# Performance work log

Hardware: AMD Instinct MI355X
Metric: run time of the kernel (lower is better)

Reference implementation:

```python
import jax, jax.numpy as jnp
import numpy as np

BN_EPS = 1e-5


def sparsemax_lastdim(z):
    # simplex projection along last axis (Martins & Astudillo 2016)
    zs = -jnp.sort(-z, axis=-1)                      # descending sort
    L = z.shape[-1]
    k = jnp.arange(1, L + 1, dtype=z.dtype)          # [L]
    cum = jnp.cumsum(zs, axis=-1)
    support = (1.0 + k * zs) > cum                   # bool [.., L]
    k_sup = jnp.sum(support, axis=-1, keepdims=True).astype(z.dtype)
    tau = (jnp.sum(jnp.where(support, zs, 0.0), axis=-1, keepdims=True) - 1.0) / k_sup
    return jnp.maximum(z - tau, 0.0)


def setup_inputs() -> dict:
    key = jax.random.key(0)
    k1, k2, k3, k4 = jax.random.split(key, 4)
    B, C_in, C_out, L, K = 16, 256, 256, 8192, 3
    x = jax.random.normal(k1, (B, C_in, L), dtype=jnp.float32)
    bn_weight = jax.random.uniform(k2, (C_in,), dtype=jnp.float32)
    bn_bias = jax.random.normal(k3, (C_in,), dtype=jnp.float32) * 0.1
    v = jax.random.normal(k4, (C_out, C_in, K), dtype=jnp.float32) * 0.05
    g = jnp.asarray(1.0, dtype=jnp.float32)  # weight_norm dim=None -> scalar gain
    return {"x": x, "bn_weight": bn_weight, "bn_bias": bn_bias, "v": v, "g": g}


def reference(x, bn_weight, bn_bias, v, g):
    # BatchNorm1d (training mode: batch statistics over batch and length)
    mean = jnp.mean(x, axis=(0, 2), keepdims=True)           # [1,C,1]
    var = jnp.mean((x - mean) ** 2, axis=(0, 2), keepdims=True)
    xn = (x - mean) * jax.lax.rsqrt(var + BN_EPS)
    xn = xn * bn_weight[None, :, None] + bn_bias[None, :, None]
    # Sparsemax over last (length) dim
    s = sparsemax_lastdim(xn)
    # weight-norm Conv1d (dim=None: scalar g over full Frobenius norm), no bias
    w = g * v / jnp.sqrt(jnp.sum(v * v))                      # [O,I,K]
    y = jax.lax.conv_general_dilated(
        s, w, window_strides=(1,), padding=[(1, 1)],
        dimension_numbers=("NCH", "OIH", "NCH"))
    # ReLU
    return jnp.maximum(y, 0.0)
```

## Files before the change

### kernel.cpp

```cpp
#include <hip/hip_runtime.h>
#include <stdint.h>
#include <math.h>

#define B_ 16
#define C_ 256
#define O_ 256
#define L_ 8192
#define NBL (B_*L_)
#define EPS_ 1e-5

typedef unsigned short ushort_t;
typedef _Float16 f16x8 __attribute__((ext_vector_type(8)));
typedef float f32x4 __attribute__((ext_vector_type(4)));

__device__ inline float wred_f(float v) {
#pragma unroll
    for (int o = 32; o > 0; o >>= 1) v += __shfl_down(v, o, 64);
    return v;
}
__device__ inline int wred_i(int v) {
#pragma unroll
    for (int o = 32; o > 0; o >>= 1) v += __shfl_down(v, o, 64);
    return v;
}
__device__ inline double wred_d(double v) {
#pragma unroll
    for (int o = 32; o > 0; o >>= 1) v += __shfl_down(v, o, 64);
    return v;
}

__device__ inline ushort_t f16bits(float x) {
    union { _Float16 h; ushort_t u; } c; c.h = (_Float16)x; return c.u;
}

__global__ __launch_bounds__(256) void k_bnpart(const float* __restrict__ x,
                                                double* __restrict__ pS,
                                                double* __restrict__ pS2) {
    const int bid = blockIdx.x;
    const int c = bid >> 2;
    const int part = bid & 3;
    const int tid = threadIdx.x;
    const int lane = tid & 63, w = tid >> 6;
    double s = 0.0, s2 = 0.0;
#pragma unroll
    for (int b = 0; b < 4; ++b) {
        const float4* p = (const float4*)(x + ((size_t)(part * 4 + b) * C_ + c) * L_);
#pragma unroll
        for (int j = 0; j < 8; ++j) {
            float4 q = p[j * 256 + tid];
            s  += (double)q.x + (double)q.y + (double)q.z + (double)q.w;
            s2 += (double)q.x * q.x + (double)q.y * q.y + (double)q.z * q.z + (double)q.w * q.w;
        }
    }
    s = wred_d(s); s2 = wred_d(s2);
    __shared__ double sv[4], sv2[4];
    if (lane == 0) { sv[w] = s; sv2[w] = s2; }
    __syncthreads();
    if (tid == 0) {
        pS[bid]  = sv[0] + sv[1] + sv[2] + sv[3];
        pS2[bid] = sv2[0] + sv2[1] + sv2[2] + sv2[3];
    }
}

__global__ __launch_bounds__(256) void k_vpart(const float* __restrict__ v,
                                               double* __restrict__ pv) {
    const int tid = threadIdx.x;
    const float4 q = ((const float4*)v)[(size_t)blockIdx.x * 256 + tid];
    double s2 = (double)q.x * q.x + (double)q.y * q.y + (double)q.z * q.z + (double)q.w * q.w;
    s2 = wred_d(s2);
    __shared__ double sv[4];
    const int lane = tid & 63, w = tid >> 6;
    if (lane == 0) sv[w] = s2;
    __syncthreads();
    if (tid == 0) pv[blockIdx.x] = sv[0] + sv[1] + sv[2] + sv[3];
}

__global__ __launch_bounds__(256) void k_finalize(const float* __restrict__ gamma,
                                                  const float* __restrict__ beta,
                                                  const float* __restrict__ g,
                                                  const double* __restrict__ pS,
                                                  const double* __restrict__ pS2,
                                                  const double* __restrict__ pv,
                                                  float* __restrict__ ab,
                                                  float* __restrict__ invn) {
    const int tid = threadIdx.x;
    const int lane = tid & 63, w = tid >> 6;
    double s2 = (tid < 192) ? pv[tid] : 0.0;
    s2 = wred_d(s2);
    __shared__ double sv[4];
    if (lane == 0) sv[w] = s2;
    __syncthreads();
    if (tid == 0) invn[0] = (float)((double)g[0] / sqrt(sv[0] + sv[1] + sv[2] + sv[3]));

    const int c = tid;
    double s  = pS[c * 4] + pS[c * 4 + 1] + pS[c * 4 + 2] + pS[c * 4 + 3];
    double ss = pS2[c * 4] + pS2[c * 4 + 1] + pS2[c * 4 + 2] + pS2[c * 4 + 3];
    const double N = (double)NBL;
    double mean = s / N;
    double var = ss / N - mean * mean;
    double rstd = 1.0 / sqrt(var + EPS_);
    double a = (double)gamma[c] * rstd;
    ab[c] = (float)a;
    ab[C_ + c] = (float)((double)beta[c] - mean * a);
}

__global__ __launch_bounds__(256) void k_wprep(const float* __restrict__ v,
                                               const float* __restrict__ invn,
                                               ushort_t* __restrict__ W,
                                               ushort_t* __restrict__ zp8) {
    const int o = blockIdx.x;
    const int c = threadIdx.x;
    const float sc = invn[0];
    if (blockIdx.x == 0) {
        for (int i = threadIdx.x; i < 4608; i += 256) zp8[i] = 0;
    }
#pragma unroll
    for (int tap = 0; tap < 3; ++tap) {
        float w = v[((size_t)o * C_ + c) * 3 + tap] * sc;
        int idx = ((tap * 16 + (o >> 4)) * 32 + (c >> 3)) * 128 + (o & 15) * 8 + (c & 7);
        W[idx] = f16bits(w);
    }
}

__global__ __launch_bounds__(256) void k_tau(const float* __restrict__ x,
                                             const float* __restrict__ ab,
                                             float* __restrict__ tauv) {
    const int row = blockIdx.x;
    const int c = row & (C_ - 1);
    const int tid = threadIdx.x;
    const int lane = tid & 63, w = tid >> 6;
    __shared__ float svf[4];
    __shared__ int svi[4];
    __shared__ float s_tau;
    __shared__ int s_cnt;

    const float a = ab[c];
    const float bb = ab[C_ + c];
    const float4* px = (const float4*)(x + (size_t)row * L_);

    float z[32];
    float sm = 0.f;
#pragma unroll
    for (int j = 0; j < 8; ++j) {
        float4 q = px[j * 256 + tid];
        float z0 = fmaf(a, q.x, bb), z1 = fmaf(a, q.y, bb);
        float z2 = fmaf(a, q.z, bb), z3 = fmaf(a, q.w, bb);
        z[4 * j] = z0; z[4 * j + 1] = z1; z[4 * j + 2] = z2; z[4 * j + 3] = z3;
        sm += z0 + z1 + z2 + z3;
    }
    sm = wred_f(sm);
    if (lane == 0) svf[w] = sm;
    __syncthreads();
    if (tid == 0) s_tau = (svf[0] + svf[1] + svf[2] + svf[3] - 1.f) * (1.f / (float)L_);
    __syncthreads();
    float tau = s_tau;
    int prev = L_;
    for (int it = 0; it < 100; ++it) {
        float ls = 0.f; int lc = 0;
#pragma unroll
        for (int j = 0; j < 32; ++j) {
            if (z[j] > tau) { ls += z[j]; ++lc; }
        }
        ls = wred_f(ls); lc = wred_i(lc);
        if (lane == 0) { svf[w] = ls; svi[w] = lc; }
        __syncthreads();
        if (tid == 0) {
            int gc = svi[0] + svi[1] + svi[2] + svi[3];
            float gs = svf[0] + svf[1] + svf[2] + svf[3];
            s_cnt = gc;
            s_tau = (gs - 1.f) / (float)gc;
        }
        __syncthreads();
        int gc = s_cnt;
        if (gc == prev) break;
        prev = gc;
        tau = s_tau;
    }
    if (tid == 0) tauv[row] = s_tau;
}

__global__ __launch_bounds__(256) void k_applyT(const float* __restrict__ x,
                                                const float* __restrict__ ab,
                                                const float* __restrict__ tauv,
                                                ushort_t* __restrict__ Sh) {
    __shared__ float sT[32 * 256];
    const int lt = blockIdx.x * 32;
    const int b = blockIdx.y;
    const int tid = threadIdx.x;
    {
        const int c = tid;
        const float a = ab[c];
        const float bb = ab[C_ + c];
        const float tv = tauv[b * C_ + c];
        const float* src = x + ((size_t)b * C_ + c) * L_ + lt;
        const int qg = c >> 2, cr = c & 3;
#pragma unroll
        for (int j = 0; j < 8; ++j) {
            float4 v4 = ((const float4*)src)[j];
            int l0 = j * 4;
            float s0 = fmaxf(fmaf(a, v4.x, bb) - tv, 0.f);
            float s1 = fmaxf(fmaf(a, v4.y, bb) - tv, 0.f);
            float s2 = fmaxf(fmaf(a, v4.z, bb) - tv, 0.f);
            float s3 = fmaxf(fmaf(a, v4.w, bb) - tv, 0.f);
            sT[(l0 + 0) * 256 + (((qg ^ ((l0 + 0) & 7)) << 2) | cr)] = s0;
            sT[(l0 + 1) * 256 + (((qg ^ ((l0 + 1) & 7)) << 2) | cr)] = s1;
            sT[(l0 + 2) * 256 + (((qg ^ ((l0 + 2) & 7)) << 2) | cr)] = s2;
            sT[(l0 + 3) * 256 + (((qg ^ ((l0 + 3) & 7)) << 2) | cr)] = s3;
        }
    }
    __syncthreads();
    const int l = tid & 31, c8 = tid >> 5;
    ushort_t hb[32];
#pragma unroll
    for (int i = 0; i < 8; ++i) {
        int qq = c8 * 8 + i;
        const float4 v4 = *(const float4*)&sT[l * 256 + ((qq ^ (l & 7)) << 2)];
        hb[i * 4 + 0] = f16bits(v4.x);
        hb[i * 4 + 1] = f16bits(v4.y);
        hb[i * 4 + 2] = f16bits(v4.z);
        hb[i * 4 + 3] = f16bits(v4.w);
    }
    const size_t tbase = (((size_t)b * 512 + ((lt + l) >> 4)) * 32) * 128 + (l & 15) * 8;
#pragma unroll
    for (int i = 0; i < 4; ++i) {
        size_t idx = tbase + (size_t)(c8 * 4 + i) * 128;
        *(uint4*)(Sh + idx) = ((const uint4*)hb)[i];
    }
}

__global__ __launch_bounds__(256) void k_sparsemax(const float* __restrict__ x,
                                                   const float* __restrict__ ab,
                                                   float* __restrict__ sout) {
    const int row = blockIdx.x;
    const int c = row & (C_ - 1);
    const int tid = threadIdx.x;
    const int lane = tid & 63, w = tid >> 6;
    __shared__ float svf[4];
    __shared__ int svi[4];
    __shared__ float s_tau;
    __shared__ int s_cnt;

    const float a = ab[c];
    const float bb = ab[C_ + c];
    const float4* px = (const float4*)(x + (size_t)row * L_);
    float4* ps = (float4*)(sout + (size_t)row * L_);

    float z[32];
    float sm = 0.f;
#pragma unroll
    for (int j = 0; j < 8; ++j) {
        float4 q = px[j * 256 + tid];
        float z0 = fmaf(a, q.x, bb), z1 = fmaf(a, q.y, bb);
        float z2 = fmaf(a, q.z, bb), z3 = fmaf(a, q.w, bb);
        z[4 * j] = z0; z[4 * j + 1] = z1; z[4 * j + 2] = z2; z[4 * j + 3] = z3;
        sm += z0 + z1 + z2 + z3;
    }
    sm = wred_f(sm);
    if (lane == 0) svf[w] = sm;
    __syncthreads();
    if (tid == 0) s_tau = (svf[0] + svf[1] + svf[2] + svf[3] - 1.f) * (1.f / (float)L_);
    __syncthreads();
    float tau = s_tau;
    int prev = L_;
    for (int it = 0; it < 100; ++it) {
        float ls = 0.f; int lc = 0;
#pragma unroll
        for (int j = 0; j < 32; ++j) {
            if (z[j] > tau) { ls += z[j]; ++lc; }
        }
        ls = wred_f(ls); lc = wred_i(lc);
        if (lane == 0) { svf[w] = ls; svi[w] = lc; }
        __syncthreads();
        if (tid == 0) {
            int gc = svi[0] + svi[1] + svi[2] + svi[3];
            float gs = svf[0] + svf[1] + svf[2] + svf[3];
            s_cnt = gc;
            s_tau = (gs - 1.f) / (float)gc;
        }
        __syncthreads();
        int gc = s_cnt;
        if (gc == prev) break;
        prev = gc;
        tau = s_tau;
    }
#pragma unroll
    for (int j = 0; j < 8; ++j) {
        float4 o;
        o.x = fmaxf(z[4 * j]     - tau, 0.f);
        o.y = fmaxf(z[4 * j + 1] - tau, 0.f);
        o.z = fmaxf(z[4 * j + 2] - tau, 0.f);
        o.w = fmaxf(z[4 * j + 3] - tau, 0.f);
        ps[j * 256 + tid] = o;
    }
}

__global__ __launch_bounds__(256) void k_transF16(const float* __restrict__ s,
                                                  ushort_t* __restrict__ Sh) {
    __shared__ float sT[32 * 256];
    const int lt = blockIdx.x * 32;
    const int b = blockIdx.y;
    const int tid = threadIdx.x;
    {
        const int c = tid;
        const float* src = s + ((size_t)b * C_ + c) * L_ + lt;
        const int qg = c >> 2, cr = c & 3;
#pragma unroll
        for (int j = 0; j < 8; ++j) {
            float4 v4 = ((const float4*)src)[j];
            int l0 = j * 4;
            sT[(l0 + 0) * 256 + (((qg ^ ((l0 + 0) & 7)) << 2) | cr)] = v4.x;
            sT[(l0 + 1) * 256 + (((qg ^ ((l0 + 1) & 7)) << 2) | cr)] = v4.y;
            sT[(l0 + 2) * 256 + (((qg ^ ((l0 + 2) & 7)) << 2) | cr)] = v4.z;
            sT[(l0 + 3) * 256 + (((qg ^ ((l0 + 3) & 7)) << 2) | cr)] = v4.w;
        }
    }
    __syncthreads();
    const int l = tid & 31, c8 = tid >> 5;
    ushort_t hb[32];
#pragma unroll
    for (int i = 0; i < 8; ++i) {
        int qq = c8 * 8 + i;
        const float4 v4 = *(const float4*)&sT[l * 256 + ((qq ^ (l & 7)) << 2)];
        hb[i * 4 + 0] = f16bits(v4.x);
        hb[i * 4 + 1] = f16bits(v4.y);
        hb[i * 4 + 2] = f16bits(v4.z);
        hb[i * 4 + 3] = f16bits(v4.w);
    }
    const size_t tbase = (((size_t)b * 512 + ((lt + l) >> 4)) * 32) * 128 + (l & 15) * 8;
#pragma unroll
    for (int i = 0; i < 4; ++i) {
        size_t idx = tbase + (size_t)(c8 * 4 + i) * 128;
        *(uint4*)(Sh + idx) = ((const uint4*)hb)[i];
    }
}

template<bool EDGE>
__device__ __forceinline__ void conv_core(const ushort_t* __restrict__ Sg,
                                          const ushort_t* __restrict__ W,
                                          const ushort_t* __restrict__ zp8,
                                          float* __restrict__ y,
                                          ushort_t* sB) {
    const int lt = blockIdx.x * 64;
    const int b = blockIdx.y;
    const int tid = threadIdx.x;
    const int wv = tid >> 6, lane = tid & 63;
    const int ml = lane & 15, qd = lane >> 4;

    const ushort_t* SgB = Sg + (size_t)b * 512 * 4096;

    {
        const ushort_t* gsrc = SgB + (size_t)(lt >> 4) * 4096;
        char* lb = (char*)sB;
#pragma unroll
        for (int it = 0; it < 8; ++it) {
            int u = it * 256 + tid;
            __builtin_amdgcn_global_load_lds(
                (const __attribute__((address_space(1))) uint32_t*)(gsrc + u * 8),
                (__attribute__((address_space(3))) uint32_t*)(lb + u * 16),
                16, 0, 0);
        }
    }

    const ushort_t* pA[3][4];
#pragma unroll
    for (int tap = 0; tap < 3; ++tap)
#pragma unroll
        for (int mi = 0; mi < 4; ++mi)
            pA[tap][mi] = W + ((tap * 16 + wv * 4 + mi) * 32 + qd) * 128 + ml * 8;

    int bOff[3][4];
#pragma unroll
    for (int tap = 0; tap < 3; ++tap)
#pragma unroll
        for (int ni = 0; ni < 4; ++ni) {
            int rc = ni * 16 + ml + tap - 1;
            int rcc = rc & 63;
            bOff[tap][ni] = ((rcc >> 4) << 13) + (qd << 8) + ((rcc & 15) << 4);
        }

    const int ccgL = lt + ml - 1;
    const int ccgR = lt + 49 + ml;
    const ushort_t* gpL;
    const ushort_t* gpR;
    {
        int cl = ccgL & (L_ - 1);
        int cr2 = ccgR & (L_ - 1);
        const ushort_t* pl = SgB + (((size_t)(cl >> 4) * 32 + qd) * 128 + (cl & 15) * 8);
        const ushort_t* pr = SgB + (((size_t)(cr2 >> 4) * 32 + qd) * 128 + (cr2 & 15) * 8);
        if (EDGE) {
            if (ccgL < 0)   pl = zp8;
            if (ccgR >= L_) pr = zp8;
        }
        gpL = pl; gpR = pr;
    }

    f32x4 acc[4][4];
#pragma unroll
    for (int mi = 0; mi < 4; ++mi)
#pragma unroll
        for (int ni = 0; ni < 4; ++ni) acc[mi][ni] = (f32x4)0.f;

    __syncthreads();

    const char* sBc = (const char*)sB;
#pragma unroll 1
    for (int ck = 0; ck < 8; ++ck) {
        const int lofs = ck * 1024;
        const int gofs = ck * 512;
#pragma unroll
        for (int tap = 0; tap < 3; ++tap) {
            f16x8 Bf[4];
#pragma unroll
            for (int ni = 0; ni < 4; ++ni) {
                if (tap == 0 && ni == 0)
                    Bf[ni] = *(const f16x8*)(gpL + gofs);
                else if (tap == 2 && ni == 3)
                    Bf[ni] = *(const f16x8*)(gpR + gofs);
                else
                    Bf[ni] = *(const f16x8*)(sBc + bOff[tap][ni] + lofs);
            }
#pragma unroll
            for (int mi = 0; mi < 4; ++mi) {
                f16x8 Af = *(const f16x8*)(pA[tap][mi] + gofs);
#pragma unroll
                for (int ni = 0; ni < 4; ++ni)
                    acc[mi][ni] = __builtin_amdgcn_mfma_f32_16x16x32_f16(Af, Bf[ni], acc[mi][ni], 0, 0, 0);
            }
        }
    }

#pragma unroll
    for (int mi = 0; mi < 4; ++mi) {
#pragma unroll
        for (int ni = 0; ni < 4; ++ni) {
            int lg = lt + ni * 16 + ml;
#pragma unroll
            for (int r = 0; r < 4; ++r) {
                int og = wv * 64 + mi * 16 + qd * 4 + r;
                y[((size_t)b * O_ + og) * L_ + lg] = fmaxf(acc[mi][ni][r], 0.f);
            }
        }
    }
}

__global__ __launch_bounds__(256, 2) void k_conv_f16(const ushort_t* __restrict__ Sg,
                                                     const ushort_t* __restrict__ W,
                                                     const ushort_t* __restrict__ zp8,
                                                     float* __restrict__ y) {
    __shared__ ushort_t sB[16384];
    if (blockIdx.x == 0 || blockIdx.x == (L_ / 64) - 1)
        conv_core<true>(Sg, W, zp8, y, sB);
    else
        conv_core<false>(Sg, W, zp8, y, sB);
}

extern "C" void kernel_launch(void* const* d_in, const int* in_sizes, int n_in,
                              void* d_out, int out_size, void* d_ws, size_t ws_size,
                              hipStream_t stream) {
    const float* x     = (const float*)d_in[0];
    const float* gamma = (const float*)d_in[1];
    const float* beta  = (const float*)d_in[2];
    const float* v     = (const float*)d_in[3];
    const float* g     = (const float*)d_in[4];
    float* y = (float*)d_out;

    char* ws = (char*)d_ws;
    float*  ab   = (float*)ws;
    float*  invn = (float*)(ws + 2048);
    double* pv   = (double*)(ws + 4096);
    double* pS   = (double*)(ws + 8192);
    double* pS2  = (double*)(ws + 16384);
    float*  tauv = (float*)(ws + 24576);
    ushort_t* W  = (ushort_t*)(ws + 49152);
    ushort_t* zp8 = (ushort_t*)(ws + 49152 + 393216);

    const size_t shOff = 1 << 20;
    const size_t need = shOff + (size_t)B_ * L_ * C_ * sizeof(ushort_t);
    const bool fast = (ws_size >= need);

    k_bnpart<<<1024, 256, 0, stream>>>(x, pS, pS2);
    k_vpart<<<192, 256, 0, stream>>>(v, pv);
    k_finalize<<<1, 256, 0, stream>>>(gamma, beta, g, pS, pS2, pv, ab, invn);
    k_wprep<<<256, 256, 0, stream>>>(v, invn, W, zp8);

    const ushort_t* Sg;
    if (fast) {
        ushort_t* Sh = (ushort_t*)(ws + shOff);
        k_tau<<<4096, 256, 0, stream>>>(x, ab, tauv);
        dim3 tg(L_ / 32, B_);
        k_applyT<<<tg, 256, 0, stream>>>(x, ab, tauv, Sh);
        Sg = Sh;
    } else {
        float* sbuf = (float*)d_out;
        ushort_t* Sh = (ushort_t*)d_in[0];
        k_sparsemax<<<4096, 256, 0, stream>>>(x, ab, sbuf);
        dim3 tg(L_ / 32, B_);
        k_transF16<<<tg, 256, 0, stream>>>(sbuf, Sh);
        Sg = Sh;
    }

    dim3 cgrid(L_ / 64, B_);
    k_conv_f16<<<cgrid, 256, 0, stream>>>(Sg, W, zp8, y);
}
```

Measured before the change: 371.1 us.

## Fuse sparsemax apply and f16 transpose into the conv kernel

Removes the separate apply/transpose kernel that wrote a full f16 transposed copy of the sparsemax output to global memory. The conv kernel now reads x directly, applies the BN affine and tau threshold, transposes through LDS into its B tile, and computes halo columns in place of the zero-padding buffer. This drops a 64 MB write plus read-back and one launch. In exchange the conv kernel uses more LDS and extra barriers, and each block recomputes the boundary columns from x.

```diff
diff --git a/kernel.cpp b/kernel.cpp
--- a/kernel.cpp
+++ b/kernel.cpp
@@ -106,14 +106,10 @@
 
 __global__ __launch_bounds__(256) void k_wprep(const float* __restrict__ v,
                                                const float* __restrict__ invn,
-                                               ushort_t* __restrict__ W,
-                                               ushort_t* __restrict__ zp8) {
+                                               ushort_t* __restrict__ W) {
     const int o = blockIdx.x;
     const int c = threadIdx.x;
     const float sc = invn[0];
-    if (blockIdx.x == 0) {
-        for (int i = threadIdx.x; i < 4608; i += 256) zp8[i] = 0;
-    }
 #pragma unroll
     for (int tap = 0; tap < 3; ++tap) {
         float w = v[((size_t)o * C_ + c) * 3 + tap] * sc;
@@ -179,185 +175,79 @@
     if (tid == 0) tauv[row] = s_tau;
 }
 
-__global__ __launch_bounds__(256) void k_applyT(const float* __restrict__ x,
-                                                const float* __restrict__ ab,
-                                                const float* __restrict__ tauv,
-                                                ushort_t* __restrict__ Sh) {
+__global__ __launch_bounds__(256, 2) void k_conv_fused(const float* __restrict__ x,
+                                                       const float* __restrict__ ab,
+                                                       const float* __restrict__ tauv,
+                                                       const ushort_t* __restrict__ W,
+                                                       float* __restrict__ y) {
+    __shared__ ushort_t sB[20480];
     __shared__ float sT[32 * 256];
-    const int lt = blockIdx.x * 32;
+
+    const int lt = blockIdx.x * 64;
     const int b = blockIdx.y;
     const int tid = threadIdx.x;
+    const int wv = tid >> 6, lane = tid & 63;
+    const int ml = lane & 15, qd = lane >> 4;
+
     {
         const int c = tid;
         const float a = ab[c];
         const float bb = ab[C_ + c];
         const float tv = tauv[b * C_ + c];
-        const float* src = x + ((size_t)b * C_ + c) * L_ + lt;
+        const float* xrow = x + ((size_t)b * C_ + c) * L_;
+
+        {
+            float sl = 0.f, sr = 0.f;
+            if (blockIdx.x != 0) {
+                float xv = xrow[lt - 1];
+                sl = fmaxf(fmaf(a, xv, bb) - tv, 0.f);
+            }
+            if (blockIdx.x != (L_ / 64) - 1) {
+                float xv = xrow[lt + 64];
+                sr = fmaxf(fmaf(a, xv, bb) - tv, 0.f);
+            }
+            ushort_t* hp = (ushort_t*)((char*)sB + 4 * 8192);
+            hp[(c >> 3) * 128 + (c & 7)]     = f16bits(sl);
+            hp[(c >> 3) * 128 + 8 + (c & 7)] = f16bits(sr);
+        }
+
         const int qg = c >> 2, cr = c & 3;
 #pragma unroll
-        for (int j = 0; j < 8; ++j) {
-            float4 v4 = ((const float4*)src)[j];
-            int l0 = j * 4;
-            float s0 = fmaxf(fmaf(a, v4.x, bb) - tv, 0.f);
-            float s1 = fmaxf(fmaf(a, v4.y, bb) - tv, 0.f);
-            float s2 = fmaxf(fmaf(a, v4.z, bb) - tv, 0.f);
-            float s3 = fmaxf(fmaf(a, v4.w, bb) - tv, 0.f);
-            sT[(l0 + 0) * 256 + (((qg ^ ((l0 + 0) & 7)) << 2) | cr)] = s0;
-            sT[(l0 + 1) * 256 + (((qg ^ ((l0 + 1) & 7)) << 2) | cr)] = s1;
-            sT[(l0 + 2) * 256 + (((qg ^ ((l0 + 2) & 7)) << 2) | cr)] = s2;
-            sT[(l0 + 3) * 256 + (((qg ^ ((l0 + 3) & 7)) << 2) | cr)] = s3;
-        }
-    }
-    __syncthreads();
-    const int l = tid & 31, c8 = tid >> 5;
-    ushort_t hb[32];
-#pragma unroll
-    for (int i = 0; i < 8; ++i) {
-        int qq = c8 * 8 + i;
-        const float4 v4 = *(const float4*)&sT[l * 256 + ((qq ^ (l & 7)) << 2)];
-        hb[i * 4 + 0] = f16bits(v4.x);
-        hb[i * 4 + 1] = f16bits(v4.y);
-        hb[i * 4 + 2] = f16bits(v4.z);
-        hb[i * 4 + 3] = f16bits(v4.w);
-    }
-    const size_t tbase = (((size_t)b * 512 + ((lt + l) >> 4)) * 32) * 128 + (l & 15) * 8;
-#pragma unroll
-    for (int i = 0; i < 4; ++i) {
-        size_t idx = tbase + (size_t)(c8 * 4 + i) * 128;
-        *(uint4*)(Sh + idx) = ((const uint4*)hb)[i];
-    }
-}
-
-__global__ __launch_bounds__(256) void k_sparsemax(const float* __restrict__ x,
-                                                   const float* __restrict__ ab,
-                                                   float* __restrict__ sout) {
-    const int row = blockIdx.x;
-    const int c = row & (C_ - 1);
-    const int tid = threadIdx.x;
-    const int lane = tid & 63, w = tid >> 6;
-    __shared__ float svf[4];
-    __shared__ int svi[4];
-    __shared__ float s_tau;
-    __shared__ int s_cnt;
-
-    const float a = ab[c];
-    const float bb = ab[C_ + c];
-    const float4* px = (const float4*)(x + (size_t)row * L_);
-    float4* ps = (float4*)(sout + (size_t)row * L_);
-
-    float z[32];
-    float sm = 0.f;
-#pragma unroll
-    for (int j = 0; j < 8; ++j) {
-        float4 q = px[j * 256 + tid];
-        float z0 = fmaf(a, q.x, bb), z1 = fmaf(a, q.y, bb);
-        float z2 = fmaf(a, q.z, bb), z3 = fmaf(a, q.w, bb);
-        z[4 * j] = z0; z[4 * j + 1] = z1; z[4 * j + 2] = z2; z[4 * j + 3] = z3;
-        sm += z0 + z1 + z2 + z3;
-    }
-    sm = wred_f(sm);
-    if (lane == 0) svf[w] = sm;
-    __syncthreads();
-    if (tid == 0) s_tau = (svf[0] + svf[1] + svf[2] + svf[3] - 1.f) * (1.f / (float)L_);
-    __syncthreads();
-    float tau = s_tau;
-    int prev = L_;
-    for (int it = 0; it < 100; ++it) {
-        float ls = 0.f; int lc = 0;
-#pragma unroll
-        for (int j = 0; j < 32; ++j) {
-            if (z[j] > tau) { ls += z[j]; ++lc; }
-        }
-        ls = wred_f(ls); lc = wred_i(lc);
-        if (lane == 0) { svf[w] = ls; svi[w] = lc; }
-        __syncthreads();
-        if (tid == 0) {
-            int gc = svi[0] + svi[1] + svi[2] + svi[3];
-            float gs = svf[0] + svf[1] + svf[2] + svf[3];
-            s_cnt = gc;
-            s_tau = (gs - 1.f) / (float)gc;
-        }
-        __syncthreads();
-        int gc = s_cnt;
-        if (gc == prev) break;
-        prev = gc;
-        tau = s_tau;
-    }
-#pragma unroll
-    for (int j = 0; j < 8; ++j) {
-        float4 o;
-        o.x = fmaxf(z[4 * j]     - tau, 0.f);
-        o.y = fmaxf(z[4 * j + 1] - tau, 0.f);
-        o.z = fmaxf(z[4 * j + 2] - tau, 0.f);
-        o.w = fmaxf(z[4 * j + 3] - tau, 0.f);
-        ps[j * 256 + tid] = o;
-    }
-}
-
-__global__ __launch_bounds__(256) void k_transF16(const float* __restrict__ s,
-                                                  ushort_t* __restrict__ Sh) {
-    __shared__ float sT[32 * 256];
-    const int lt = blockIdx.x * 32;
-    const int b = blockIdx.y;
-    const int tid = threadIdx.x;
-    {
-        const int c = tid;
-        const float* src = s + ((size_t)b * C_ + c) * L_ + lt;
-        const int qg = c >> 2, cr = c & 3;
-#pragma unroll
-        for (int j = 0; j < 8; ++j) {
-            float4 v4 = ((const float4*)src)[j];
-            int l0 = j * 4;
-            sT[(l0 + 0) * 256 + (((qg ^ ((l0 + 0) & 7)) << 2) | cr)] = v4.x;
-            sT[(l0 + 1) * 256 + (((qg ^ ((l0 + 1) & 7)) << 2) | cr)] = v4.y;
-            sT[(l0 + 2) * 256 + (((qg ^ ((l0 + 2) & 7)) << 2) | cr)] = v4.z;
-            sT[(l0 + 3) * 256 + (((qg ^ ((l0 + 3) & 7)) << 2) | cr)] = v4.w;
-        }
-    }
-    __syncthreads();
-    const int l = tid & 31, c8 = tid >> 5;
-    ushort_t hb[32];
-#pragma unroll
-    for (int i = 0; i < 8; ++i) {
-        int qq = c8 * 8 + i;
-        const float4 v4 = *(const float4*)&sT[l * 256 + ((qq ^ (l & 7)) << 2)];
-        hb[i * 4 + 0] = f16bits(v4.x);
-        hb[i * 4 + 1] = f16bits(v4.y);
-        hb[i * 4 + 2] = f16bits(v4.z);
-        hb[i * 4 + 3] = f16bits(v4.w);
-    }
-    const size_t tbase = (((size_t)b * 512 + ((lt + l) >> 4)) * 32) * 128 + (l & 15) * 8;
-#pragma unroll
-    for (int i = 0; i < 4; ++i) {
-        size_t idx = tbase + (size_t)(c8 * 4 + i) * 128;
-        *(uint4*)(Sh + idx) = ((const uint4*)hb)[i];
-    }
-}
-
-template<bool EDGE>
-__device__ __forceinline__ void conv_core(const ushort_t* __restrict__ Sg,
-                                          const ushort_t* __restrict__ W,
-                                          const ushort_t* __restrict__ zp8,
-                                          float* __restrict__ y,
-                                          ushort_t* sB) {
-    const int lt = blockIdx.x * 64;
-    const int b = blockIdx.y;
-    const int tid = threadIdx.x;
-    const int wv = tid >> 6, lane = tid & 63;
-    const int ml = lane & 15, qd = lane >> 4;
-
-    const ushort_t* SgB = Sg + (size_t)b * 512 * 4096;
-
-    {
-        const ushort_t* gsrc = SgB + (size_t)(lt >> 4) * 4096;
-        char* lb = (char*)sB;
-#pragma unroll
-        for (int it = 0; it < 8; ++it) {
-            int u = it * 256 + tid;
-            __builtin_amdgcn_global_load_lds(
-                (const __attribute__((address_space(1))) uint32_t*)(gsrc + u * 8),
-                (__attribute__((address_space(3))) uint32_t*)(lb + u * 16),
-                16, 0, 0);
+        for (int p = 0; p < 2; ++p) {
+            const float4* src = (const float4*)(xrow + lt + p * 32);
+#pragma unroll
+            for (int j = 0; j < 8; ++j) {
+                float4 v4 = src[j];
+                int l0 = j * 4;
+                float s0 = fmaxf(fmaf(a, v4.x, bb) - tv, 0.f);
+                float s1 = fmaxf(fmaf(a, v4.y, bb) - tv, 0.f);
+                float s2 = fmaxf(fmaf(a, v4.z, bb) - tv, 0.f);
+                float s3 = fmaxf(fmaf(a, v4.w, bb) - tv, 0.f);
+                sT[(l0 + 0) * 256 + (((qg ^ ((l0 + 0) & 7)) << 2) | cr)] = s0;
+                sT[(l0 + 1) * 256 + (((qg ^ ((l0 + 1) & 7)) << 2) | cr)] = s1;
+                sT[(l0 + 2) * 256 + (((qg ^ ((l0 + 2) & 7)) << 2) | cr)] = s2;
+                sT[(l0 + 3) * 256 + (((qg ^ ((l0 + 3) & 7)) << 2) | cr)] = s3;
+            }
+            __syncthreads();
+            {
+                const int l = tid & 31, c8 = tid >> 5;
+                ushort_t hb[32];
+#pragma unroll
+                for (int i = 0; i < 8; ++i) {
+                    int qq = c8 * 8 + i;
+                    const float4 v4 = *(const float4*)&sT[l * 256 + ((qq ^ (l & 7)) << 2)];
+                    hb[i * 4 + 0] = f16bits(v4.x);
+                    hb[i * 4 + 1] = f16bits(v4.y);
+                    hb[i * 4 + 2] = f16bits(v4.z);
+                    hb[i * 4 + 3] = f16bits(v4.w);
+                }
+                const int ll = p * 32 + l;
+                char* dst = (char*)sB + (ll >> 4) * 8192 + (ll & 15) * 16;
+#pragma unroll
+                for (int i = 0; i < 4; ++i)
+                    *(uint4*)(dst + (c8 * 4 + i) * 256) = ((const uint4*)hb)[i];
+            }
+            __syncthreads();
         }
     }
 
@@ -374,33 +264,18 @@
 #pragma unroll
         for (int ni = 0; ni < 4; ++ni) {
             int rc = ni * 16 + ml + tap - 1;
-            int rcc = rc & 63;
-            bOff[tap][ni] = ((rcc >> 4) << 13) + (qd << 8) + ((rcc & 15) << 4);
-        }
-
-    const int ccgL = lt + ml - 1;
-    const int ccgR = lt + 49 + ml;
-    const ushort_t* gpL;
-    const ushort_t* gpR;
-    {
-        int cl = ccgL & (L_ - 1);
-        int cr2 = ccgR & (L_ - 1);
-        const ushort_t* pl = SgB + (((size_t)(cl >> 4) * 32 + qd) * 128 + (cl & 15) * 8);
-        const ushort_t* pr = SgB + (((size_t)(cr2 >> 4) * 32 + qd) * 128 + (cr2 & 15) * 8);
-        if (EDGE) {
-            if (ccgL < 0)   pl = zp8;
-            if (ccgR >= L_) pr = zp8;
-        }
-        gpL = pl; gpR = pr;
-    }
+            int o;
+            if (rc < 0)       o = 4 * 8192 + (qd << 8);
+            else if (rc > 63) o = 4 * 8192 + (qd << 8) + 16;
+            else              o = ((rc >> 4) << 13) + (qd << 8) + ((rc & 15) << 4);
+            bOff[tap][ni] = o;
+        }
 
     f32x4 acc[4][4];
 #pragma unroll
     for (int mi = 0; mi < 4; ++mi)
 #pragma unroll
         for (int ni = 0; ni < 4; ++ni) acc[mi][ni] = (f32x4)0.f;
-
-    __syncthreads();
 
     const char* sBc = (const char*)sB;
 #pragma unroll 1
@@ -411,14 +286,8 @@
         for (int tap = 0; tap < 3; ++tap) {
             f16x8 Bf[4];
 #pragma unroll
-            for (int ni = 0; ni < 4; ++ni) {
-                if (tap == 0 && ni == 0)
-                    Bf[ni] = *(const f16x8*)(gpL + gofs);
-                else if (tap == 2 && ni == 3)
-                    Bf[ni] = *(const f16x8*)(gpR + gofs);
-                else
-                    Bf[ni] = *(const f16x8*)(sBc + bOff[tap][ni] + lofs);
-            }
+            for (int ni = 0; ni < 4; ++ni)
+                Bf[ni] = *(const f16x8*)(sBc + bOff[tap][ni] + lofs);
 #pragma unroll
             for (int mi = 0; mi < 4; ++mi) {
                 f16x8 Af = *(const f16x8*)(pA[tap][mi] + gofs);
@@ -441,17 +310,6 @@
             }
         }
     }
-}
-
-__global__ __launch_bounds__(256, 2) void k_conv_f16(const ushort_t* __restrict__ Sg,
-                                                     const ushort_t* __restrict__ W,
-                                                     const ushort_t* __restrict__ zp8,
-                                                     float* __restrict__ y) {
-    __shared__ ushort_t sB[16384];
-    if (blockIdx.x == 0 || blockIdx.x == (L_ / 64) - 1)
-        conv_core<true>(Sg, W, zp8, y, sB);
-    else
-        conv_core<false>(Sg, W, zp8, y, sB);
 }
 
 extern "C" void kernel_launch(void* const* d_in, const int* in_sizes, int n_in,
@@ -472,33 +330,13 @@
     double* pS2  = (double*)(ws + 16384);
     float*  tauv = (float*)(ws + 24576);
     ushort_t* W  = (ushort_t*)(ws + 49152);
-    ushort_t* zp8 = (ushort_t*)(ws + 49152 + 393216);
-
-    const size_t shOff = 1 << 20;
-    const size_t need = shOff + (size_t)B_ * L_ * C_ * sizeof(ushort_t);
-    const bool fast = (ws_size >= need);
 
     k_bnpart<<<1024, 256, 0, stream>>>(x, pS, pS2);
     k_vpart<<<192, 256, 0, stream>>>(v, pv);
     k_finalize<<<1, 256, 0, stream>>>(gamma, beta, g, pS, pS2, pv, ab, invn);
-    k_wprep<<<256, 256, 0, stream>>>(v, invn, W, zp8);
-
-    const ushort_t* Sg;
-    if (fast) {
-        ushort_t* Sh = (ushort_t*)(ws + shOff);
-        k_tau<<<4096, 256, 0, stream>>>(x, ab, tauv);
-        dim3 tg(L_ / 32, B_);
-        k_applyT<<<tg, 256, 0, stream>>>(x, ab, tauv, Sh);
-        Sg = Sh;
-    } else {
-        float* sbuf = (float*)d_out;
-        ushort_t* Sh = (ushort_t*)d_in[0];
-        k_sparsemax<<<4096, 256, 0, stream>>>(x, ab, sbuf);
-        dim3 tg(L_ / 32, B_);
-        k_transF16<<<tg, 256, 0, stream>>>(sbuf, Sh);
-        Sg = Sh;
-    }
+    k_wprep<<<256, 256, 0, stream>>>(v, invn, W);
+    k_tau<<<4096, 256, 0, stream>>>(x, ab, tauv);
 
     dim3 cgrid(L_ / 64, B_);
-    k_conv_f16<<<cgrid, 256, 0, stream>>>(Sg, W, zp8, y);
-}
+    k_conv_fused<<<cgrid, 256, 0, stream>>>(x, ab, tauv, W, y);
+}
```

After: 387.9 us. 4.5% more time.

## Cut tau-iteration barriers with double-buffered reductions; tune conv unroll and occupancy

Applied to the files above, without the earlier changes.

The sparsemax threshold loop now lets every thread compute tau redundantly from double-buffered shared partials. This removes the second __syncthreads and the single-thread serial step in each iteration. Counts are reduced as floats so one shuffle-reduction routine covers both sums. Separately, the conv inner loop is unrolled by 2 and launch bounds ask for 3 blocks per SM, which adds register pressure and a risk of spills in exchange for more occupancy.

```diff
diff --git a/kernel.cpp b/kernel.cpp
--- a/kernel.cpp
+++ b/kernel.cpp
@@ -129,10 +129,8 @@
     const int c = row & (C_ - 1);
     const int tid = threadIdx.x;
     const int lane = tid & 63, w = tid >> 6;
-    __shared__ float svf[4];
-    __shared__ int svi[4];
-    __shared__ float s_tau;
-    __shared__ int s_cnt;
+    __shared__ float svf[2][4];
+    __shared__ float svc[2][4];
 
     const float a = ab[c];
     const float bb = ab[C_ + c];
@@ -149,34 +147,29 @@
         sm += z0 + z1 + z2 + z3;
     }
     sm = wred_f(sm);
-    if (lane == 0) svf[w] = sm;
-    __syncthreads();
-    if (tid == 0) s_tau = (svf[0] + svf[1] + svf[2] + svf[3] - 1.f) * (1.f / (float)L_);
-    __syncthreads();
-    float tau = s_tau;
+    if (lane == 0) svf[0][w] = sm;
+    __syncthreads();
+    float tau = (svf[0][0] + svf[0][1] + svf[0][2] + svf[0][3] - 1.f) * (1.f / (float)L_);
     int prev = L_;
+#pragma unroll 1
     for (int it = 0; it < 100; ++it) {
-        float ls = 0.f; int lc = 0;
+        float ls = 0.f, lc = 0.f;
 #pragma unroll
         for (int j = 0; j < 32; ++j) {
-            if (z[j] > tau) { ls += z[j]; ++lc; }
-        }
-        ls = wred_f(ls); lc = wred_i(lc);
-        if (lane == 0) { svf[w] = ls; svi[w] = lc; }
+            if (z[j] > tau) { ls += z[j]; lc += 1.f; }
+        }
+        ls = wred_f(ls); lc = wred_f(lc);
+        const int pb = (it & 1) ^ 1;
+        if (lane == 0) { svf[pb][w] = ls; svc[pb][w] = lc; }
         __syncthreads();
-        if (tid == 0) {
-            int gc = svi[0] + svi[1] + svi[2] + svi[3];
-            float gs = svf[0] + svf[1] + svf[2] + svf[3];
-            s_cnt = gc;
-            s_tau = (gs - 1.f) / (float)gc;
-        }
-        __syncthreads();
-        int gc = s_cnt;
-        if (gc == prev) break;
-        prev = gc;
-        tau = s_tau;
-    }
-    if (tid == 0) tauv[row] = s_tau;
+        float gs = svf[pb][0] + svf[pb][1] + svf[pb][2] + svf[pb][3];
+        float gc = svc[pb][0] + svc[pb][1] + svc[pb][2] + svc[pb][3];
+        tau = (gs - 1.f) / gc;
+        int gci = (int)gc;
+        if (gci == prev) break;
+        prev = gci;
+    }
+    if (tid == 0) tauv[row] = tau;
 }
 
 __global__ __launch_bounds__(256) void k_applyT(const float* __restrict__ x,
@@ -403,7 +396,7 @@
     __syncthreads();
 
     const char* sBc = (const char*)sB;
-#pragma unroll 1
+#pragma unroll 2
     for (int ck = 0; ck < 8; ++ck) {
         const int lofs = ck * 1024;
         const int gofs = ck * 512;
@@ -443,7 +436,7 @@
     }
 }
 
-__global__ __launch_bounds__(256, 2) void k_conv_f16(const ushort_t* __restrict__ Sg,
+__global__ __launch_bounds__(256, 3) void k_conv_f16(const ushort_t* __restrict__ Sg,
                                                      const ushort_t* __restrict__ W,
                                                      const ushort_t* __restrict__ zp8,
                                                      float* __restrict__ y) {
```

New measurement: 409.1 us. 1.1x slower.
